# Performance work log

Hardware: AMD Instinct MI355X
Metric: run time of the kernel (lower is better)

The kernel has to match this reference:

```python
import math
import jax, jax.numpy as jnp
import numpy as np

BATCH, SEQ, D_MODEL, NUM_HEADS = 4, 2048, 1024, 16
D_K = D_MODEL // NUM_HEADS


def setup_inputs() -> dict:
    key = jax.random.key(0)
    ks = jax.random.split(key, 11)
    s = 0.02
    inp = {
        'encodings_q': jax.random.normal(ks[0], (BATCH, SEQ, D_MODEL), jnp.float32),
        'encodings_k': jax.random.normal(ks[1], (BATCH, SEQ, D_MODEL), jnp.float32),
        'encodings_v': jax.random.normal(ks[2], (BATCH, SEQ, D_MODEL), jnp.float32),
        # causal mask: True = masked out (matches masked_fill semantics)
        'mask': jnp.broadcast_to(jnp.triu(jnp.ones((SEQ, SEQ), bool), k=1),
                                 (BATCH, SEQ, SEQ)),
        'Wq': jax.random.normal(ks[3], (D_MODEL, D_MODEL), jnp.float32) * s,
        'bq': jnp.zeros((D_MODEL,), jnp.float32),
        'Wk': jax.random.normal(ks[4], (D_MODEL, D_MODEL), jnp.float32) * s,
        'bk': jnp.zeros((D_MODEL,), jnp.float32),
        'Wv': jax.random.normal(ks[5], (D_MODEL, D_MODEL), jnp.float32) * s,
        'bv': jnp.zeros((D_MODEL,), jnp.float32),
        'Wo': jax.random.normal(ks[6], (D_MODEL, D_MODEL), jnp.float32) * s,
        'bo': jnp.zeros((D_MODEL,), jnp.float32),
    }
    return inp


def reference(encodings_q, encodings_k, encodings_v, mask,
              Wq, bq, Wk, bk, Wv, bv, Wo, bo):
    B, S, D = encodings_q.shape
    H, Dk = NUM_HEADS, D_K
    # projections (nn.Linear: x @ W.T + b), split heads -> (B, H, S, Dk)
    q = (encodings_q @ Wq.T + bq).reshape(B, S, H, Dk).transpose(0, 2, 1, 3)
    k = (encodings_k @ Wk.T + bk).reshape(B, S, H, Dk).transpose(0, 2, 1, 3)
    v = (encodings_v @ Wv.T + bv).reshape(B, S, H, Dk).transpose(0, 2, 1, 3)
    scores = jnp.einsum('bhqd,bhkd->bhqk', q, k) / math.sqrt(Dk)
    # mask dim == 3 -> unsqueeze head dim; masked_fill(mask, -1e9)
    scores = jnp.where(mask[:, None, :, :], jnp.float32(-1e9), scores)
    weights = jax.nn.softmax(scores, axis=-1)
    attn = jnp.einsum('bhqk,bhkd->bhqd', weights, v)
    attn = attn.transpose(0, 2, 1, 3).reshape(B, S, D)
    return attn @ Wo.T + bo
```

## Files before the change

### kernel.cpp

```cpp
#include <hip/hip_runtime.h>
#include <hip/hip_bf16.h>
#include <cstdint>

typedef __bf16 bf16;
typedef bf16  bf16x4 __attribute__((ext_vector_type(4)));
typedef bf16  bf16x8 __attribute__((ext_vector_type(8)));
typedef float f32x4  __attribute__((ext_vector_type(4)));

#define MFMA16(a, b, c) __builtin_amdgcn_mfma_f32_16x16x32_bf16((a), (b), (c), 0, 0, 0)

constexpr int BATCH = 4;
constexpr int SEQ   = 2048;
constexpr int DM    = 1024;
constexpr int NH    = 16;
constexpr int DK    = 64;

__device__ __forceinline__ void gld_lds16(const void* g, void* l) {
    __builtin_amdgcn_global_load_lds(
        (const __attribute__((address_space(1))) unsigned int*)(uintptr_t)g,
        (__attribute__((address_space(3))) unsigned int*)(uintptr_t)l,
        16, 0, 0);
}

__device__ __forceinline__ bf16x8 cvt8(const float* __restrict__ p) {
    f32x4 a = *(const f32x4*)p;
    f32x4 b = *(const f32x4*)(p + 4);
    bf16x8 r;
    r[0] = (bf16)a[0]; r[1] = (bf16)a[1]; r[2] = (bf16)a[2]; r[3] = (bf16)a[3];
    r[4] = (bf16)b[0]; r[5] = (bf16)b[1]; r[6] = (bf16)b[2]; r[7] = (bf16)b[3];
    return r;
}

__global__ __launch_bounds__(256)
void cvt_x3(const float* __restrict__ s0, const float* __restrict__ s1,
            const float* __restrict__ s2, bf16* __restrict__ dst) {
    const float* s = (blockIdx.y == 0) ? s0 : (blockIdx.y == 1) ? s1 : s2;
    const size_t i = ((size_t)blockIdx.x * 256 + threadIdx.x) * 8;
    *(bf16x8*)(dst + (size_t)blockIdx.y * ((size_t)BATCH * SEQ * DM) + i) = cvt8(s + i);
}

__global__ __launch_bounds__(256)
void cvt_x(const float* __restrict__ src, bf16* __restrict__ dst) {
    const size_t i = ((size_t)blockIdx.x * 256 + threadIdx.x) * 8;
    *(bf16x8*)(dst + i) = cvt8(src + i);
}

__global__ __launch_bounds__(256)
void cvt_w4(const float* __restrict__ s0, const float* __restrict__ s1,
            const float* __restrict__ s2, const float* __restrict__ s3,
            bf16* __restrict__ dst) {
    const float* s = (blockIdx.y == 0) ? s0 : (blockIdx.y == 1) ? s1
                   : (blockIdx.y == 2) ? s2 : s3;
    const size_t i = ((size_t)blockIdx.x * 256 + threadIdx.x) * 8;
    *(bf16x8*)(dst + (size_t)blockIdx.y * (1024 * 1024) + i) = cvt8(s + i);
}

__device__ __forceinline__
void gemm_core(const bf16* __restrict__ A, const bf16* __restrict__ W,
               const float* __restrict__ bias, void* __restrict__ outp,
               int mode, int m0, int n0, bf16* As, bf16* Bs)
{
    const int tid  = threadIdx.x;
    const int lane = tid & 63;
    const int wave = tid >> 6;
    const int wm   = (wave >> 1) * 64;
    const int wn   = (wave & 1) * 64;
    const int q    = lane >> 4;
    const int r    = lane & 15;
    const int srow = lane >> 2;
    const int scol = (lane & 3) * 8;

    f32x4 acc[4][4];
#pragma unroll
    for (int i = 0; i < 4; i++)
#pragma unroll
        for (int j = 0; j < 4; j++) acc[i][j] = (f32x4){0.f, 0.f, 0.f, 0.f};

    const bf16* Ag = A + (size_t)(m0 + wave * 32 + srow) * 1024 + scol;
    const bf16* Wg = W + (size_t)(n0 + wave * 32 + srow) * 1024 + scol;
    bf16* AsB = &As[(wave * 32) * 32];
    bf16* BsB = &Bs[(wave * 32) * 32];

    for (int k0 = 0; k0 < 1024; k0 += 32) {
        __syncthreads();
        gld_lds16(Ag + k0,             AsB);
        gld_lds16(Ag + 16 * 1024 + k0, AsB + 16 * 32);
        gld_lds16(Wg + k0,             BsB);
        gld_lds16(Wg + 16 * 1024 + k0, BsB + 16 * 32);
        __syncthreads();

        bf16x8 af[4], bfr[4];
#pragma unroll
        for (int i = 0; i < 4; i++)
            af[i] = *(const bf16x8*)&As[(wm + i * 16 + r) * 32 + q * 8];
#pragma unroll
        for (int j = 0; j < 4; j++)
            bfr[j] = *(const bf16x8*)&Bs[(wn + j * 16 + r) * 32 + q * 8];
#pragma unroll
        for (int i = 0; i < 4; i++)
#pragma unroll
            for (int j = 0; j < 4; j++)
                acc[i][j] = MFMA16(af[i], bfr[j], acc[i][j]);
    }

#pragma unroll
    for (int j = 0; j < 4; j++) {
        const int col = n0 + wn + j * 16 + r;
        const float bv = bias[col];
#pragma unroll
        for (int i = 0; i < 4; i++) {
#pragma unroll
            for (int rr = 0; rr < 4; rr++) {
                const int row = m0 + wm + i * 16 + q * 4 + rr;
                const float v = acc[i][j][rr] + bv;
                if (mode == 1) {
                    ((float*)outp)[(size_t)row * 1024 + col] = v;
                } else {
                    const int b = row >> 11, s = row & 2047;
                    const int hh = col >> 6, d = col & 63;
                    if (mode == 0)
                        ((bf16*)outp)[(((size_t)(b * NH + hh)) * SEQ + s) * DK + d] = (bf16)v;
                    else
                        ((bf16*)outp)[(((size_t)(b * NH + hh)) * DK + d) * SEQ + s] = (bf16)v;
                }
            }
        }
    }
}

template <int MODE>
__global__ __launch_bounds__(256)
void gemm_fast(const bf16* __restrict__ A, const bf16* __restrict__ W,
               const float* __restrict__ bias, void* __restrict__ outp)
{
    __shared__ __align__(16) bf16 As[128 * 32];
    __shared__ __align__(16) bf16 Bs[128 * 32];
    gemm_core(A, W, bias, outp, MODE, blockIdx.y * 128, blockIdx.x * 128, As, Bs);
}

__global__ __launch_bounds__(256)
void gemm_qkv(const bf16* __restrict__ X3, const bf16* __restrict__ WB,
              const float* __restrict__ bq, const float* __restrict__ bk,
              const float* __restrict__ bv,
              bf16* __restrict__ Qt, bf16* __restrict__ Kt, bf16* __restrict__ Vt)
{
    __shared__ __align__(16) bf16 As[128 * 32];
    __shared__ __align__(16) bf16 Bs[128 * 32];
    const int z = blockIdx.z;
    const size_t E = (size_t)BATCH * SEQ * DM, WE = (size_t)DM * DM;
    const bf16* A = X3 + (size_t)z * E;
    const bf16* W = WB + (size_t)z * WE;
    const float* bias = (z == 0) ? bq : (z == 1) ? bk : bv;
    void* outp = (z == 0) ? (void*)Qt : (z == 1) ? (void*)Kt : (void*)Vt;
    gemm_core(A, W, bias, outp, (z == 2) ? 2 : 0,
              blockIdx.y * 128, blockIdx.x * 128, As, Bs);
}

template <int MODE>
__global__ __launch_bounds__(256)
void gemm_slow(const void* __restrict__ Ap, const float* __restrict__ W,
               const float* __restrict__ bias, void* __restrict__ outp)
{
    __shared__ __align__(16) bf16 As[128 * 32];
    __shared__ __align__(16) bf16 Bs[128 * 32];

    const int tid  = threadIdx.x;
    const int lane = tid & 63;
    const int wave = tid >> 6;
    const int wm   = (wave >> 1) * 64;
    const int wn   = (wave & 1) * 64;
    const int m0   = blockIdx.y * 128;
    const int n0   = blockIdx.x * 128;
    const int q    = lane >> 4;
    const int r    = lane & 15;
    const int lrow  = tid >> 2;
    const int lcol8 = (tid & 3) * 8;

    f32x4 acc[4][4];
#pragma unroll
    for (int i = 0; i < 4; i++)
#pragma unroll
        for (int j = 0; j < 4; j++) acc[i][j] = (f32x4){0.f, 0.f, 0.f, 0.f};

    for (int k0 = 0; k0 < 1024; k0 += 32) {
        __syncthreads();
        if (MODE != 1) {
            const float* Af = (const float*)Ap;
            *(bf16x8*)&As[lrow * 32 + lcol8] =
                cvt8(&Af[(size_t)(m0 + lrow) * 1024 + k0 + lcol8]);
            *(bf16x8*)&As[(64 + lrow) * 32 + lcol8] =
                cvt8(&Af[(size_t)(m0 + 64 + lrow) * 1024 + k0 + lcol8]);
        } else {
            const bf16* Ab = (const bf16*)Ap;
            *(bf16x8*)&As[lrow * 32 + lcol8] =
                *(const bf16x8*)&Ab[(size_t)(m0 + lrow) * 1024 + k0 + lcol8];
            *(bf16x8*)&As[(64 + lrow) * 32 + lcol8] =
                *(const bf16x8*)&Ab[(size_t)(m0 + 64 + lrow) * 1024 + k0 + lcol8];
        }
        *(bf16x8*)&Bs[lrow * 32 + lcol8] =
            cvt8(&W[(size_t)(n0 + lrow) * 1024 + k0 + lcol8]);
        *(bf16x8*)&Bs[(64 + lrow) * 32 + lcol8] =
            cvt8(&W[(size_t)(n0 + 64 + lrow) * 1024 + k0 + lcol8]);
        __syncthreads();

        bf16x8 af[4], bfr[4];
#pragma unroll
        for (int i = 0; i < 4; i++)
            af[i] = *(const bf16x8*)&As[(wm + i * 16 + r) * 32 + q * 8];
#pragma unroll
        for (int j = 0; j < 4; j++)
            bfr[j] = *(const bf16x8*)&Bs[(wn + j * 16 + r) * 32 + q * 8];
#pragma unroll
        for (int i = 0; i < 4; i++)
#pragma unroll
            for (int j = 0; j < 4; j++)
                acc[i][j] = MFMA16(af[i], bfr[j], acc[i][j]);
    }

#pragma unroll
    for (int j = 0; j < 4; j++) {
        const int col = n0 + wn + j * 16 + r;
        const float bv = bias[col];
#pragma unroll
        for (int i = 0; i < 4; i++) {
#pragma unroll
            for (int rr = 0; rr < 4; rr++) {
                const int row = m0 + wm + i * 16 + q * 4 + rr;
                const float v = acc[i][j][rr] + bv;
                if (MODE == 1) {
                    ((float*)outp)[(size_t)row * 1024 + col] = v;
                } else {
                    const int b = row >> 11, s = row & 2047;
                    const int hh = col >> 6, d = col & 63;
                    if (MODE == 0)
                        ((bf16*)outp)[(((size_t)(b * NH + hh)) * SEQ + s) * DK + d] = (bf16)v;
                    else
                        ((bf16*)outp)[(((size_t)(b * NH + hh)) * DK + d) * SEQ + s] = (bf16)v;
                }
            }
        }
    }
}

__global__ __launch_bounds__(256)
void attn_causal(const bf16* __restrict__ Qt, const bf16* __restrict__ Kt,
                 const bf16* __restrict__ Vtt, bf16* __restrict__ Ob)
{
    constexpr int LDK = 72;
    __shared__ __align__(16) bf16 Ks[64 * LDK];
    __shared__ __align__(16) bf16 Vs[64 * LDK];
    __shared__ __align__(16) bf16 Ps[4][16 * LDK];

    const int tid  = threadIdx.x;
    const int lane = tid & 63;
    const int wave = tid >> 6;
    const int q4   = lane >> 4;
    const int r    = lane & 15;

    const int bh = blockIdx.x;
    const int qb = blockIdx.y * 64;
    const int b  = bh >> 4;
    const int h  = bh & 15;

    const bf16* Qp = Qt  + ((size_t)bh * SEQ + qb + wave * 16) * DK;
    const bf16* Kp = Kt  + (size_t)bh * SEQ * DK;
    const bf16* Vp = Vtt + (size_t)bh * DK * SEQ;

    bf16x8 qf0 = *(const bf16x8*)&Qp[r * DK + q4 * 8];
    bf16x8 qf1 = *(const bf16x8*)&Qp[r * DK + 32 + q4 * 8];
#pragma unroll
    for (int j = 0; j < 8; j++) {
        qf0[j] = (bf16)((float)qf0[j] * 0.125f);
        qf1[j] = (bf16)((float)qf1[j] * 0.125f);
    }

    bf16x8 ones;
#pragma unroll
    for (int j = 0; j < 8; j++) ones[j] = (bf16)1.0f;

    f32x4 o[4], o5;
#pragma unroll
    for (int i = 0; i < 4; i++) o[i] = (f32x4){0.f, 0.f, 0.f, 0.f};
    o5 = (f32x4){0.f, 0.f, 0.f, 0.f};
    float m_i = -1e30f;

    const int nT   = blockIdx.y + 1;
    const int lrow = tid >> 2;
    const int lcol = (tid & 3) * 16;
    const int qrow = qb + wave * 16 + r;

    for (int t = 0; t < nT; ++t) {
        const int kb = t * 64;
        __syncthreads();
        *(bf16x8*)&Ks[lrow * LDK + lcol] =
            *(const bf16x8*)&Kp[(size_t)(kb + lrow) * DK + lcol];
        *(bf16x8*)&Ks[lrow * LDK + lcol + 8] =
            *(const bf16x8*)&Kp[(size_t)(kb + lrow) * DK + lcol + 8];
        *(bf16x8*)&Vs[lrow * LDK + lcol] =
            *(const bf16x8*)&Vp[(size_t)lrow * SEQ + kb + lcol];
        *(bf16x8*)&Vs[lrow * LDK + lcol + 8] =
            *(const bf16x8*)&Vp[(size_t)lrow * SEQ + kb + lcol + 8];
        __syncthreads();

        f32x4 s[4];
#pragma unroll
        for (int n = 0; n < 4; n++) {
            bf16x8 k0 = *(const bf16x8*)&Ks[(n * 16 + r) * LDK + q4 * 8];
            bf16x8 k1 = *(const bf16x8*)&Ks[(n * 16 + r) * LDK + 32 + q4 * 8];
            f32x4 a = (f32x4){0.f, 0.f, 0.f, 0.f};
            a = MFMA16(k0, qf0, a);
            a = MFMA16(k1, qf1, a);
            s[n] = a;
        }

        float mx = -1e30f;
        if (t == nT - 1) {
#pragma unroll
            for (int n = 0; n < 4; n++) {
                const int c0 = kb + n * 16 + q4 * 4;
#pragma unroll
                for (int rr = 0; rr < 4; rr++) {
                    if (c0 + rr > qrow) s[n][rr] = -1e30f;
                    mx = fmaxf(mx, s[n][rr]);
                }
            }
        } else {
#pragma unroll
            for (int n = 0; n < 4; n++)
#pragma unroll
                for (int rr = 0; rr < 4; rr++)
                    mx = fmaxf(mx, s[n][rr]);
        }
        mx = fmaxf(mx, __shfl_xor(mx, 16, 64));
        mx = fmaxf(mx, __shfl_xor(mx, 32, 64));

        const float mn = fmaxf(m_i, mx);
        const float alpha = __expf(m_i - mn);
        m_i = mn;
#pragma unroll
        for (int n = 0; n < 4; n++)
#pragma unroll
            for (int rr = 0; rr < 4; rr++)
                o[n][rr] *= alpha;
#pragma unroll
        for (int rr = 0; rr < 4; rr++) o5[rr] *= alpha;

        bf16* Pw = &Ps[wave][0];
#pragma unroll
        for (int n = 0; n < 4; n++) {
            bf16x4 pv;
#pragma unroll
            for (int rr = 0; rr < 4; rr++)
                pv[rr] = (bf16)__expf(s[n][rr] - m_i);
            *(bf16x4*)&Pw[r * LDK + n * 16 + q4 * 4] = pv;
        }
        asm volatile("s_waitcnt lgkmcnt(0)" ::: "memory");

#pragma unroll
        for (int kk = 0; kk < 2; kk++) {
            bf16x8 pf = *(const bf16x8*)&Pw[r * LDK + kk * 32 + q4 * 8];
#pragma unroll
            for (int n = 0; n < 4; n++) {
                bf16x8 vf = *(const bf16x8*)&Vs[(n * 16 + r) * LDK + kk * 32 + q4 * 8];
                o[n] = MFMA16(vf, pf, o[n]);
            }
            o5 = MFMA16(ones, pf, o5);
        }
    }

    const float inv = 1.0f / o5[0];
#pragma unroll
    for (int n = 0; n < 4; n++) {
        bf16x4 ov;
#pragma unroll
        for (int rr = 0; rr < 4; rr++) ov[rr] = (bf16)(o[n][rr] * inv);
        *(bf16x4*)&Ob[((size_t)b * SEQ + qrow) * DM + h * DK + n * 16 + q4 * 4] = ov;
    }
}

extern "C" void kernel_launch(void* const* d_in, const int* in_sizes, int n_in,
                              void* d_out, int out_size, void* d_ws, size_t ws_size,
                              hipStream_t stream)
{
    const float* xq = (const float*)d_in[0];
    const float* xk = (const float*)d_in[1];
    const float* xv = (const float*)d_in[2];
    const float* Wq = (const float*)d_in[4];
    const float* bq = (const float*)d_in[5];
    const float* Wk = (const float*)d_in[6];
    const float* bk = (const float*)d_in[7];
    const float* Wv = (const float*)d_in[8];
    const float* bv = (const float*)d_in[9];
    const float* Wo = (const float*)d_in[10];
    const float* bo = (const float*)d_in[11];

    const size_t E  = (size_t)BATCH * SEQ * DM;
    const size_t WE = (size_t)DM * DM;
    bf16* Qt = (bf16*)d_ws;
    bf16* Kt = Qt + E;
    bf16* Vt = Kt + E;
    bf16* Ab = Vt + E;

    dim3 gblk(256);
    dim3 ggrid(DM / 128, (BATCH * SEQ) / 128);
    dim3 agrid(BATCH * NH, SEQ / 64);

    const size_t need_fused = (7 * E + 4 * WE) * sizeof(bf16);
    const size_t need_fast  = (5 * E + 4 * WE) * sizeof(bf16);

    if (ws_size >= need_fused) {
        bf16* X3 = Ab + E;
        bf16* WB = X3 + 3 * E;

        cvt_w4<<<dim3(512, 4), gblk, 0, stream>>>(Wq, Wk, Wv, Wo, WB);
        cvt_x3<<<dim3(4096, 3), gblk, 0, stream>>>(xq, xk, xv, X3);

        gemm_qkv<<<dim3(8, 64, 3), gblk, 0, stream>>>(X3, WB, bq, bk, bv, Qt, Kt, Vt);

        attn_causal<<<agrid, gblk, 0, stream>>>(Qt, Kt, Vt, Ab);

        gemm_fast<1><<<ggrid, gblk, 0, stream>>>(Ab, WB + 3 * WE, bo, d_out);
    } else if (ws_size >= need_fast) {
        bf16* X  = Ab + E;
        bf16* WB = X + E;

        cvt_w4<<<dim3(512, 4), gblk, 0, stream>>>(Wq, Wk, Wv, Wo, WB);

        cvt_x<<<dim3(4096), gblk, 0, stream>>>(xq, X);
        gemm_fast<0><<<ggrid, gblk, 0, stream>>>(X, WB + 0 * WE, bq, Qt);
        cvt_x<<<dim3(4096), gblk, 0, stream>>>(xk, X);
        gemm_fast<0><<<ggrid, gblk, 0, stream>>>(X, WB + 1 * WE, bk, Kt);
        cvt_x<<<dim3(4096), gblk, 0, stream>>>(xv, X);
        gemm_fast<2><<<ggrid, gblk, 0, stream>>>(X, WB + 2 * WE, bv, Vt);

        attn_causal<<<agrid, gblk, 0, stream>>>(Qt, Kt, Vt, Ab);

        gemm_fast<1><<<ggrid, gblk, 0, stream>>>(Ab, WB + 3 * WE, bo, d_out);
    } else {
        gemm_slow<0><<<ggrid, gblk, 0, stream>>>(xq, Wq, bq, Qt);
        gemm_slow<0><<<ggrid, gblk, 0, stream>>>(xk, Wk, bk, Kt);
        gemm_slow<2><<<ggrid, gblk, 0, stream>>>(xv, Wv, bv, Vt);
        attn_causal<<<agrid, gblk, 0, stream>>>(Qt, Kt, Vt, Ab);
        gemm_slow<1><<<ggrid, gblk, 0, stream>>>(Ab, Wo, bo, d_out);
    }
}
```

Before: 401.6 us.

## Vectorize GEMM epilogue stores via swapped MFMA operands, merge conversion kernels, reorder grid

For Q/K and output modes the MFMA operands are swapped so each lane holds four consecutive columns. The epilogue can then write bf16x4 or f32x4 vectors, with a vector bias load, instead of scalar strided stores. For V the transposed layout already gives consecutive sequence positions per lane, so it also writes bf16x4. The two conversion launches are merged into one kernel, and the GEMM grid is reordered so blockIdx.x walks M tiles, which changes L2 reuse of weight and activation tiles.

New measurement: 373.9 us. 6.9% less time.

```diff
diff --git a/kernel.cpp b/kernel.cpp
--- a/kernel.cpp
+++ b/kernel.cpp
@@ -32,11 +32,30 @@
 }
 
 __global__ __launch_bounds__(256)
-void cvt_x3(const float* __restrict__ s0, const float* __restrict__ s1,
-            const float* __restrict__ s2, bf16* __restrict__ dst) {
-    const float* s = (blockIdx.y == 0) ? s0 : (blockIdx.y == 1) ? s1 : s2;
-    const size_t i = ((size_t)blockIdx.x * 256 + threadIdx.x) * 8;
-    *(bf16x8*)(dst + (size_t)blockIdx.y * ((size_t)BATCH * SEQ * DM) + i) = cvt8(s + i);
+void cvt_all(const float* __restrict__ xq, const float* __restrict__ xk,
+             const float* __restrict__ xv,
+             const float* __restrict__ wq, const float* __restrict__ wk,
+             const float* __restrict__ wv, const float* __restrict__ wo,
+             bf16* __restrict__ X3, bf16* __restrict__ WB)
+{
+    const int bid = blockIdx.x;
+    const float* s;
+    bf16* d;
+    int local;
+    if (bid < 12288) {
+        const int which = bid >> 12;
+        local = bid & 4095;
+        s = (which == 0) ? xq : (which == 1) ? xk : xv;
+        d = X3 + (size_t)which * ((size_t)BATCH * SEQ * DM);
+    } else {
+        const int b2 = bid - 12288;
+        const int which = b2 >> 9;
+        local = b2 & 511;
+        s = (which == 0) ? wq : (which == 1) ? wk : (which == 2) ? wv : wo;
+        d = WB + (size_t)which * (size_t)(DM * DM);
+    }
+    const size_t i = ((size_t)local * 256 + threadIdx.x) * 8;
+    *(bf16x8*)(d + i) = cvt8(s + i);
 }
 
 __global__ __launch_bounds__(256)
@@ -55,17 +74,18 @@
     *(bf16x8*)(dst + (size_t)blockIdx.y * (1024 * 1024) + i) = cvt8(s + i);
 }
 
+template <int MODE>
 __device__ __forceinline__
 void gemm_core(const bf16* __restrict__ A, const bf16* __restrict__ W,
                const float* __restrict__ bias, void* __restrict__ outp,
-               int mode, int m0, int n0, bf16* As, bf16* Bs)
+               int m0, int n0, bf16* As, bf16* Bs)
 {
     const int tid  = threadIdx.x;
     const int lane = tid & 63;
     const int wave = tid >> 6;
     const int wm   = (wave >> 1) * 64;
     const int wn   = (wave & 1) * 64;
-    const int q    = lane >> 4;
+    const int q4   = lane >> 4;
     const int r    = lane & 15;
     const int srow = lane >> 2;
     const int scol = (lane & 3) * 8;
@@ -92,36 +112,55 @@
         bf16x8 af[4], bfr[4];
 #pragma unroll
         for (int i = 0; i < 4; i++)
-            af[i] = *(const bf16x8*)&As[(wm + i * 16 + r) * 32 + q * 8];
+            af[i] = *(const bf16x8*)&As[(wm + i * 16 + r) * 32 + q4 * 8];
 #pragma unroll
         for (int j = 0; j < 4; j++)
-            bfr[j] = *(const bf16x8*)&Bs[(wn + j * 16 + r) * 32 + q * 8];
+            bfr[j] = *(const bf16x8*)&Bs[(wn + j * 16 + r) * 32 + q4 * 8];
 #pragma unroll
         for (int i = 0; i < 4; i++)
 #pragma unroll
-            for (int j = 0; j < 4; j++)
-                acc[i][j] = MFMA16(af[i], bfr[j], acc[i][j]);
-    }
-
-#pragma unroll
-    for (int j = 0; j < 4; j++) {
-        const int col = n0 + wn + j * 16 + r;
-        const float bv = bias[col];
-#pragma unroll
-        for (int i = 0; i < 4; i++) {
-#pragma unroll
-            for (int rr = 0; rr < 4; rr++) {
-                const int row = m0 + wm + i * 16 + q * 4 + rr;
-                const float v = acc[i][j][rr] + bv;
-                if (mode == 1) {
-                    ((float*)outp)[(size_t)row * 1024 + col] = v;
+            for (int j = 0; j < 4; j++) {
+                if (MODE == 2)
+                    acc[i][j] = MFMA16(af[i], bfr[j], acc[i][j]);
+                else
+                    acc[i][j] = MFMA16(bfr[j], af[i], acc[i][j]);
+            }
+    }
+
+    if (MODE == 2) {
+#pragma unroll
+        for (int j = 0; j < 4; j++) {
+            const int col = n0 + wn + j * 16 + r;
+            const float bv = bias[col];
+            const int hh = col >> 6, d = col & 63;
+#pragma unroll
+            for (int i = 0; i < 4; i++) {
+                const int s0 = m0 + wm + i * 16 + q4 * 4;
+                const int b = s0 >> 11, s = s0 & 2047;
+                bf16x4 ov;
+#pragma unroll
+                for (int rr = 0; rr < 4; rr++) ov[rr] = (bf16)(acc[i][j][rr] + bv);
+                *(bf16x4*)&((bf16*)outp)[(((size_t)(b * NH + hh)) * DK + d) * SEQ + s] = ov;
+            }
+        }
+    } else {
+#pragma unroll
+        for (int j = 0; j < 4; j++) {
+            const int col0 = n0 + wn + j * 16 + q4 * 4;
+            const f32x4 bv4 = *(const f32x4*)&bias[col0];
+#pragma unroll
+            for (int i = 0; i < 4; i++) {
+                const int row = m0 + wm + i * 16 + r;
+                if (MODE == 1) {
+                    f32x4 ov = acc[i][j] + bv4;
+                    *(f32x4*)&((float*)outp)[(size_t)row * 1024 + col0] = ov;
                 } else {
                     const int b = row >> 11, s = row & 2047;
-                    const int hh = col >> 6, d = col & 63;
-                    if (mode == 0)
-                        ((bf16*)outp)[(((size_t)(b * NH + hh)) * SEQ + s) * DK + d] = (bf16)v;
-                    else
-                        ((bf16*)outp)[(((size_t)(b * NH + hh)) * DK + d) * SEQ + s] = (bf16)v;
+                    const int hh = col0 >> 6, d0 = col0 & 63;
+                    bf16x4 ov;
+#pragma unroll
+                    for (int rr = 0; rr < 4; rr++) ov[rr] = (bf16)(acc[i][j][rr] + bv4[rr]);
+                    *(bf16x4*)&((bf16*)outp)[(((size_t)(b * NH + hh)) * SEQ + s) * DK + d0] = ov;
                 }
             }
         }
@@ -135,7 +174,7 @@
 {
     __shared__ __align__(16) bf16 As[128 * 32];
     __shared__ __align__(16) bf16 Bs[128 * 32];
-    gemm_core(A, W, bias, outp, MODE, blockIdx.y * 128, blockIdx.x * 128, As, Bs);
+    gemm_core<MODE>(A, W, bias, outp, blockIdx.x * 128, blockIdx.y * 128, As, Bs);
 }
 
 __global__ __launch_bounds__(256)
@@ -150,10 +189,13 @@
     const size_t E = (size_t)BATCH * SEQ * DM, WE = (size_t)DM * DM;
     const bf16* A = X3 + (size_t)z * E;
     const bf16* W = WB + (size_t)z * WE;
-    const float* bias = (z == 0) ? bq : (z == 1) ? bk : bv;
-    void* outp = (z == 0) ? (void*)Qt : (z == 1) ? (void*)Kt : (void*)Vt;
-    gemm_core(A, W, bias, outp, (z == 2) ? 2 : 0,
-              blockIdx.y * 128, blockIdx.x * 128, As, Bs);
+    const int m0 = blockIdx.x * 128, n0 = blockIdx.y * 128;
+    if (z == 2)
+        gemm_core<2>(A, W, bv, Vt, m0, n0, As, Bs);
+    else if (z == 1)
+        gemm_core<0>(A, W, bk, Kt, m0, n0, As, Bs);
+    else
+        gemm_core<0>(A, W, bq, Qt, m0, n0, As, Bs);
 }
 
 template <int MODE>
@@ -402,7 +444,6 @@
     bf16* Ab = Vt + E;
 
     dim3 gblk(256);
-    dim3 ggrid(DM / 128, (BATCH * SEQ) / 128);
     dim3 agrid(BATCH * NH, SEQ / 64);
 
     const size_t need_fused = (7 * E + 4 * WE) * sizeof(bf16);
@@ -412,14 +453,13 @@
         bf16* X3 = Ab + E;
         bf16* WB = X3 + 3 * E;
 
-        cvt_w4<<<dim3(512, 4), gblk, 0, stream>>>(Wq, Wk, Wv, Wo, WB);
-        cvt_x3<<<dim3(4096, 3), gblk, 0, stream>>>(xq, xk, xv, X3);
-
-        gemm_qkv<<<dim3(8, 64, 3), gblk, 0, stream>>>(X3, WB, bq, bk, bv, Qt, Kt, Vt);
+        cvt_all<<<dim3(14336), gblk, 0, stream>>>(xq, xk, xv, Wq, Wk, Wv, Wo, X3, WB);
+
+        gemm_qkv<<<dim3(64, 8, 3), gblk, 0, stream>>>(X3, WB, bq, bk, bv, Qt, Kt, Vt);
 
         attn_causal<<<agrid, gblk, 0, stream>>>(Qt, Kt, Vt, Ab);
 
-        gemm_fast<1><<<ggrid, gblk, 0, stream>>>(Ab, WB + 3 * WE, bo, d_out);
+        gemm_fast<1><<<dim3(64, 8), gblk, 0, stream>>>(Ab, WB + 3 * WE, bo, d_out);
     } else if (ws_size >= need_fast) {
         bf16* X  = Ab + E;
         bf16* WB = X + E;
@@ -427,20 +467,21 @@
         cvt_w4<<<dim3(512, 4), gblk, 0, stream>>>(Wq, Wk, Wv, Wo, WB);
 
         cvt_x<<<dim3(4096), gblk, 0, stream>>>(xq, X);
-        gemm_fast<0><<<ggrid, gblk, 0, stream>>>(X, WB + 0 * WE, bq, Qt);
+        gemm_fast<0><<<dim3(64, 8), gblk, 0, stream>>>(X, WB + 0 * WE, bq, Qt);
         cvt_x<<<dim3(4096), gblk, 0, stream>>>(xk, X);
-        gemm_fast<0><<<ggrid, gblk, 0, stream>>>(X, WB + 1 * WE, bk, Kt);
+        gemm_fast<0><<<dim3(64, 8), gblk, 0, stream>>>(X, WB + 1 * WE, bk, Kt);
         cvt_x<<<dim3(4096), gblk, 0, stream>>>(xv, X);
-        gemm_fast<2><<<ggrid, gblk, 0, stream>>>(X, WB + 2 * WE, bv, Vt);
+        gemm_fast<2><<<dim3(64, 8), gblk, 0, stream>>>(X, WB + 2 * WE, bv, Vt);
 
         attn_causal<<<agrid, gblk, 0, stream>>>(Qt, Kt, Vt, Ab);
 
-        gemm_fast<1><<<ggrid, gblk, 0, stream>>>(Ab, WB + 3 * WE, bo, d_out);
+        gemm_fast<1><<<dim3(64, 8), gblk, 0, stream>>>(Ab, WB + 3 * WE, bo, d_out);
     } else {
-        gemm_slow<0><<<ggrid, gblk, 0, stream>>>(xq, Wq, bq, Qt);
-        gemm_slow<0><<<ggrid, gblk, 0, stream>>>(xk, Wk, bk, Kt);
-        gemm_slow<2><<<ggrid, gblk, 0, stream>>>(xv, Wv, bv, Vt);
+        dim3 ggrid_s(DM / 128, (BATCH * SEQ) / 128);
+        gemm_slow<0><<<ggrid_s, gblk, 0, stream>>>(xq, Wq, bq, Qt);
+        gemm_slow<0><<<ggrid_s, gblk, 0, stream>>>(xk, Wk, bk, Kt);
+        gemm_slow<2><<<ggrid_s, gblk, 0, stream>>>(xv, Wv, bv, Vt);
         attn_causal<<<agrid, gblk, 0, stream>>>(Qt, Kt, Vt, Ab);
-        gemm_slow<1><<<ggrid, gblk, 0, stream>>>(Ab, Wo, bo, d_out);
-    }
-}
+        gemm_slow<1><<<ggrid_s, gblk, 0, stream>>>(Ab, Wo, bo, d_out);
+    }
+}
```
